# Kernel optimization log

Measured on AMD Instinct MI355X. Metric: run time of the kernel, lower is better.

The kernel has to match this reference:

```python
import jax, jax.numpy as jnp
import numpy as np

T, B, X, H, Z = 28, 16384, 28, 100, 16
EPS = 1e-10


def setup_inputs() -> dict:
    key = jax.random.key(0)
    ks = jax.random.split(key, 32)
    s = 0.1  # weight scale to keep activations sane
    d = {
        'x': jax.random.uniform(ks[0], (T, B, X), jnp.float32),
        'eps': jax.random.normal(ks[1], (T, B, Z), jnp.float32),
        'Wpx': jax.random.normal(ks[2], (H, X)) * s, 'bpx': jnp.zeros((H,)),
        'Wpz': jax.random.normal(ks[3], (H, Z)) * s, 'bpz': jnp.zeros((H,)),
        'Wp1': jax.random.normal(ks[4], (H, H)) * s, 'bp1': jnp.zeros((H,)),
        'Wp_mu': jax.random.normal(ks[5], (Z, H)) * s, 'bp_mu': jnp.zeros((Z,)),
        'Wp_sig': jax.random.normal(ks[6], (Z, H)) * s, 'bp_sig': jnp.zeros((Z,)),
        'We1': jax.random.normal(ks[7], (H, 2 * H)) * s, 'be1': jnp.zeros((H,)),
        'We_mu': jax.random.normal(ks[8], (Z, H)) * s, 'be_mu': jnp.zeros((Z,)),
        'We_sig': jax.random.normal(ks[9], (Z, H)) * s, 'be_sig': jnp.zeros((Z,)),
        'Wd1': jax.random.normal(ks[10], (H, 2 * H)) * s, 'bd1': jnp.zeros((H,)),
        'Wd2': jax.random.normal(ks[11], (H, H)) * s, 'bd2': jnp.zeros((H,)),
        'Wd3': jax.random.normal(ks[12], (X, H)) * s, 'bd3': jnp.zeros((X,)),
        'Wih': jax.random.normal(ks[13], (3 * H, 2 * H)) * s, 'Whh': jax.random.normal(ks[14], (3 * H, H)) * s,
        'bih': jnp.zeros((3 * H,)), 'bhh': jnp.zeros((3 * H,)),
    }
    return {k: v.astype(jnp.float32) for k, v in d.items()}


def _lin(a, W, b):
    return a @ W.T + b


def reference(x, eps, Wpx, bpx, Wpz, bpz, Wp1, bp1, Wp_mu, bp_mu, Wp_sig, bp_sig,
              We1, be1, We_mu, be_mu, We_sig, be_sig, Wd1, bd1, Wd2, bd2, Wd3, bd3,
              Wih, Whh, bih, bhh):
    def step(h, inp):
        xt, et = inp  # [B,X], [B,Z]
        px = jax.nn.relu(_lin(xt, Wpx, bpx))  # phi_x
        # encoder q(z|x,h)
        he = jax.nn.relu(_lin(jnp.concatenate([px, h], -1), We1, be1))
        enc_mu = _lin(he, We_mu, be_mu)
        enc_sig = jax.nn.softplus(_lin(he, We_sig, be_sig))
        # prior p(z|h)
        hp = jax.nn.relu(_lin(h, Wp1, bp1))
        pr_mu = _lin(hp, Wp_mu, bp_mu)
        pr_sig = jax.nn.softplus(_lin(hp, Wp_sig, bp_sig))
        # reparameterize (torch code uses sqrt(scale) -- treat scale as var)
        z = enc_mu + jnp.sqrt(enc_sig) * et
        pz = jax.nn.relu(_lin(z, Wpz, bpz))  # phi_z
        # decoder p(x|z,h)
        hd = jax.nn.relu(_lin(jnp.concatenate([pz, h], -1), Wd1, bd1))
        hd = jax.nn.relu(_lin(hd, Wd2, bd2))
        probs = jax.nn.sigmoid(_lin(hd, Wd3, bd3))
        # GRUCell(input=[pz, px], h)
        gi = jnp.concatenate([pz, px], -1) @ Wih.T + bih
        gh = h @ Whh.T + bhh
        ir, iu, in_ = jnp.split(gi, 3, -1)
        hr, hu, hn = jnp.split(gh, 3, -1)
        r = jax.nn.sigmoid(ir + hr)
        u = jax.nn.sigmoid(iu + hu)
        n = jnp.tanh(in_ + r * hn)
        h_next = (1.0 - u) * n + u * h
        # KL(enc || prior)
        ps = pr_sig + EPS
        kl = 0.5 * (2 * jnp.log(ps) - 2 * jnp.log(enc_sig)
                    + (enc_sig ** 2 + (enc_mu - pr_mu) ** 2) / ps ** 2 - 1.0)
        kl = kl.sum(1).mean()
        # Bernoulli NLL
        nll = -(xt * jnp.log(probs + EPS) + (1.0 - xt) * jnp.log(1.0 - probs + EPS))
        nll = nll.sum(1).mean()
        return h_next, (kl, nll)

    h0 = jnp.zeros((x.shape[1], H), x.dtype)
    _, (kls, nlls) = jax.lax.scan(step, h0, (x, eps))
    return kls.sum(), nlls.sum()
```

## Files before the change

### kernel.cpp

```cpp
#include <hip/hip_runtime.h>
#include <math.h>

#define DEVFN __device__ __forceinline__

namespace {

typedef __bf16 bf16x8 __attribute__((ext_vector_type(8)));
typedef float  f32x4  __attribute__((ext_vector_type(4)));

constexpr int T = 28, B = 16384, X = 28, H = 100, Z = 16;
constexpr int ROWS = 32;
constexpr int NTH  = 256;
constexpr int ST   = 104;
constexpr int HBUF = ROWS*ST + 24;
constexpr int XST  = 40;
constexpr float KEPS = 1e-10f;

constexpr int FB_PX   = 0;
constexpr int FB_HE   = 7;
constexpr int FB_EMU  = 63;
constexpr int FB_ESIG = 67;
constexpr int FB_HP   = 71;
constexpr int FB_PMU  = 99;
constexpr int FB_PSIG = 103;
constexpr int FB_PZ   = 107;
constexpr int FB_HD1  = 114;
constexpr int FB_HD2  = 170;
constexpr int FB_PRB  = 198;
constexpr int FB_GIR  = 206;
constexpr int FB_GIU  = 262;
constexpr int FB_GIN  = 318;
constexpr int FB_GHR  = 374;
constexpr int FB_GHU  = 402;
constexpr int FB_GHN  = 430;
constexpr int NFRAG   = 458;

struct Params {
  const float *x,*eps,*Wpx,*bpx,*Wpz,*bpz,*Wp1,*bp1,*Wp_mu,*bp_mu,*Wp_sig,*bp_sig,
              *We1,*be1,*We_mu,*be_mu,*We_sig,*be_sig,*Wd1,*bd1,*Wd2,*bd2,*Wd3,*bd3,
              *Wih,*Whh,*bih,*bhh;
  float *out;
};

DEVFN float frcp(float x){ return __builtin_amdgcn_rcpf(x); }
DEVFN float fsigmoid(float v){ return frcp(1.f + __expf(-v)); }
DEVFN float ftanh(float v){
  float t = __expf(-2.f*fabsf(v));
  float r = (1.f - t) * frcp(1.f + t);
  return copysignf(r, v);
}
DEVFN float fsoftplus(float v){
  float sp = (v > 15.f) ? v : __logf(1.f + __expf(v));
  return fmaxf(sp, 1e-6f);
}

DEVFN f32x4 MFMA(bf16x8 a, bf16x8 b, f32x4 c){
  return __builtin_amdgcn_mfma_f32_16x16x32_bf16(a, b, c, 0, 0, 0);
}

__global__ void prep_kernel(Params P, __bf16* FRW)
{
  const int f = blockIdx.x, l = threadIdx.x;
  const int bases[18] = {FB_PX,FB_HE,FB_EMU,FB_ESIG,FB_HP,FB_PMU,FB_PSIG,FB_PZ,FB_HD1,
                         FB_HD2,FB_PRB,FB_GIR,FB_GIU,FB_GIN,FB_GHR,FB_GHU,FB_GHN,NFRAG};
  int li = 0;
  while (f >= bases[li+1]) ++li;

  const float* W; const float* Bv; int KT, N, roff, wstr, vK, mode;
  switch (li) {
    case 0:  W=P.Wpx;    Bv=P.bpx;    KT=1; N=100; roff=0;   wstr=28;  vK=28;  mode=0; break;
    case 1:  W=P.We1;    Bv=P.be1;    KT=8; N=100; roff=0;   wstr=200; vK=100; mode=1; break;
    case 2:  W=P.We_mu;  Bv=P.be_mu;  KT=4; N=16;  roff=0;   wstr=100; vK=100; mode=0; break;
    case 3:  W=P.We_sig; Bv=P.be_sig; KT=4; N=16;  roff=0;   wstr=100; vK=100; mode=0; break;
    case 4:  W=P.Wp1;    Bv=P.bp1;    KT=4; N=100; roff=0;   wstr=100; vK=100; mode=0; break;
    case 5:  W=P.Wp_mu;  Bv=P.bp_mu;  KT=4; N=16;  roff=0;   wstr=100; vK=100; mode=0; break;
    case 6:  W=P.Wp_sig; Bv=P.bp_sig; KT=4; N=16;  roff=0;   wstr=100; vK=100; mode=0; break;
    case 7:  W=P.Wpz;    Bv=P.bpz;    KT=1; N=100; roff=0;   wstr=16;  vK=16;  mode=0; break;
    case 8:  W=P.Wd1;    Bv=P.bd1;    KT=8; N=100; roff=0;   wstr=200; vK=100; mode=1; break;
    case 9:  W=P.Wd2;    Bv=P.bd2;    KT=4; N=100; roff=0;   wstr=100; vK=100; mode=0; break;
    case 10: W=P.Wd3;    Bv=P.bd3;    KT=4; N=28;  roff=0;   wstr=100; vK=100; mode=0; break;
    case 11: W=P.Wih;    Bv=P.bih;    KT=8; N=100; roff=0;   wstr=200; vK=100; mode=1; break;
    case 12: W=P.Wih;    Bv=P.bih;    KT=8; N=100; roff=100; wstr=200; vK=100; mode=1; break;
    case 13: W=P.Wih;    Bv=P.bih;    KT=8; N=100; roff=200; wstr=200; vK=100; mode=1; break;
    case 14: W=P.Whh;    Bv=P.bhh;    KT=4; N=100; roff=0;   wstr=100; vK=100; mode=0; break;
    case 15: W=P.Whh;    Bv=P.bhh;    KT=4; N=100; roff=100; wstr=100; vK=100; mode=0; break;
    default: W=P.Whh;    Bv=P.bhh;    KT=4; N=100; roff=200; wstr=100; vK=100; mode=0; break;
  }
  const int idx = f - bases[li];
  const int nt = idx / KT, kc = idx % KT;
  const int n  = nt*16 + (l & 15);

  bf16x8 v;
  #pragma unroll
  for (int j = 0; j < 8; ++j) {
    int kk  = (mode ? (kc & 3) : kc)*32 + ((l >> 4)*8) + j;
    float w = 0.f;
    if (n < N) {
      if (mode == 0) {
        if (kk < vK)       w = W[(size_t)(roff + n)*wstr + kk];
        else if (kk == vK) w = Bv[roff + n];
      } else {
        int col = (kc < 4 ? 0 : 100) + kk;
        if (kk < 100)                    w = W[(size_t)(roff + n)*wstr + col];
        else if (kc < 4 && kk == 100)    w = Bv[roff + n];
      }
    }
    v[j] = (__bf16)w;
  }
  *((bf16x8*)FRW + (size_t)f*64 + l) = v;
}

template<int NC>
DEVFN void load_afrags2(bf16x8 (&af)[2][NC], const __bf16* A, int stride, int lane)
{
  #pragma unroll
  for (int mh = 0; mh < 2; ++mh) {
    const __bf16* p = A + (size_t)((lane & 15) + mh*16)*stride + ((lane >> 4)*8);
    #pragma unroll
    for (int kc = 0; kc < NC; ++kc) af[mh][kc] = *(const bf16x8*)(p + kc*32);
  }
}

DEVFN bf16x8 vload_frag(const __bf16* A, int stride, int mh, int kc, int lane)
{
  const __bf16* p = A + (size_t)((lane & 15) + mh*16)*stride + ((lane >> 4)*8) + kc*32;
  return *(const volatile bf16x8*)p;
}

template<int KT>
DEVFN void layerH2(const bf16x8 (&af)[2][KT], const bf16x8* FRbase, __bf16* dst, int sw, int step, int lane)
{
  for (int nt = sw; nt < 7; nt += step) {
    f32x4 ac0 = {0.f,0.f,0.f,0.f}, ac1 = {0.f,0.f,0.f,0.f};
    const bf16x8* wf = FRbase + (size_t)nt*KT*64 + lane;
    #pragma unroll
    for (int kc = 0; kc < KT; ++kc) {
      bf16x8 w = wf[kc*64];
      ac0 = MFMA(af[0][kc], w, ac0);
      ac1 = MFMA(af[1][kc], w, ac1);
    }
    const int col = nt*16 + (lane & 15);
    if (col < H) {
      const int rbase = (lane >> 4)*4;
      #pragma unroll
      for (int r = 0; r < 4; ++r) {
        dst[(size_t)(rbase + r)*ST + col]      = (__bf16)fmaxf(ac0[r], 0.f);
        dst[(size_t)(16 + rbase + r)*ST + col] = (__bf16)fmaxf(ac1[r], 0.f);
      }
    }
  }
}

DEVFN void layerHcat2_1(const bf16x8 (&b0)[2][4], const bf16x8 (&b1)[2][4], const bf16x8* FRbase,
                        __bf16* dst, int nt, int lane)
{
  f32x4 ac0 = {0.f,0.f,0.f,0.f}, ac1 = {0.f,0.f,0.f,0.f};
  const bf16x8* wf = FRbase + (size_t)nt*8*64 + lane;
  #pragma unroll
  for (int kc = 0; kc < 4; ++kc) {
    bf16x8 w = wf[kc*64];
    ac0 = MFMA(b0[0][kc], w, ac0);
    ac1 = MFMA(b0[1][kc], w, ac1);
  }
  #pragma unroll
  for (int kc = 0; kc < 4; ++kc) {
    bf16x8 w = wf[(4+kc)*64];
    ac0 = MFMA(b1[0][kc], w, ac0);
    ac1 = MFMA(b1[1][kc], w, ac1);
  }
  const int col = nt*16 + (lane & 15);
  if (col < H) {
    const int rbase = (lane >> 4)*4;
    #pragma unroll
    for (int r = 0; r < 4; ++r) {
      dst[(size_t)(rbase + r)*ST + col]      = (__bf16)fmaxf(ac0[r], 0.f);
      dst[(size_t)(16 + rbase + r)*ST + col] = (__bf16)fmaxf(ac1[r], 0.f);
    }
  }
}

template<int KT>
DEVFN void head4x2(const bf16x8 (&af)[2][KT], const bf16x8* FRbase, int lane, f32x4& o0, f32x4& o1)
{
  f32x4 ac0 = {0.f,0.f,0.f,0.f}, ac1 = {0.f,0.f,0.f,0.f};
  #pragma unroll
  for (int kc = 0; kc < KT; ++kc) {
    bf16x8 w = FRbase[kc*64 + lane];
    ac0 = MFMA(af[0][kc], w, ac0);
    ac1 = MFMA(af[1][kc], w, ac1);
  }
  o0 = ac0; o1 = ac1;
}

template<int KT>
DEVFN f32x4 head4(const bf16x8 (&af)[KT], const bf16x8* FRbase, int lane)
{
  f32x4 acc = {0.f,0.f,0.f,0.f};
  #pragma unroll
  for (int kc = 0; kc < KT; ++kc) acc = MFMA(af[kc], FRbase[kc*64 + lane], acc);
  return acc;
}

__global__ __launch_bounds__(NTH, 2) void vrnn_kernel(Params P, const __bf16* FRW)
{
  __shared__ alignas(16) __bf16 sPXb[2][HBUF];
  __shared__ alignas(16) __bf16 sPZ[HBUF];
  __shared__ alignas(16) __bf16 sA [HBUF];
  __shared__ alignas(16) __bf16 sBb[2][HBUF];
  __shared__ alignas(16) __bf16 sH0[HBUF];
  __shared__ alignas(16) __bf16 sH1[HBUF];
  __shared__ alignas(16) __bf16 sZ [ROWS*XST];
  __shared__ float sred[8];

  const bf16x8* FR = (const bf16x8*)FRW;
  const int tid  = threadIdx.x;
  const int lane = tid & 63;
  const int uwv  = __builtin_amdgcn_readfirstlane(tid >> 6);
  const int gr0  = blockIdx.x * ROWS;

  for (int i = tid; i < HBUF; i += NTH) {
    sPXb[0][i]=(__bf16)0.f; sPXb[1][i]=(__bf16)0.f; sPZ[i]=(__bf16)0.f; sA[i]=(__bf16)0.f;
    sBb[0][i]=(__bf16)0.f; sBb[1][i]=(__bf16)0.f; sH0[i]=(__bf16)0.f; sH1[i]=(__bf16)0.f;
  }
  for (int i = tid; i < ROWS*XST; i += NTH) sZ[i]=(__bf16)0.f;
  __syncthreads();
  if (tid < ROWS) {
    sPXb[0][tid*ST+100]=(__bf16)1.f; sPXb[1][tid*ST+100]=(__bf16)1.f;
    sPZ[tid*ST+100]=(__bf16)1.f; sA[tid*ST+100]=(__bf16)1.f;
    sBb[0][tid*ST+100]=(__bf16)1.f; sBb[1][tid*ST+100]=(__bf16)1.f;
    sH0[tid*ST+100]=(__bf16)1.f; sH1[tid*ST+100]=(__bf16)1.f;
    sZ[tid*XST+16]=(__bf16)1.f;
  }
  __syncthreads();

  float kl = 0.f, nll = 0.f;

  for (int t = 0; t < T; ++t) {
    __bf16* sHo = (t & 1) ? sH1 : sH0;
    __bf16* sHn = (t & 1) ? sH0 : sH1;
    __bf16* sPX = sPXb[t & 1];
    __bf16* sB  = sBb [t & 1];

    {
      bf16x8 ax[2][1];
      #pragma unroll
      for (int mh = 0; mh < 2; ++mh) {
        const float* xr = P.x + ((size_t)t*B + gr0 + mh*16 + (lane & 15))*X + (lane >> 4)*8;
        float4 fa = *(const float4*)xr;
        float4 fb = make_float4(0.f,0.f,0.f,0.f);
        if ((lane >> 4) < 3) fb = *(const float4*)(xr + 4);
        bf16x8 a;
        a[0]=(__bf16)fa.x; a[1]=(__bf16)fa.y; a[2]=(__bf16)fa.z; a[3]=(__bf16)fa.w;
        a[4]=(__bf16)fb.x; a[5]=(__bf16)fb.y; a[6]=(__bf16)fb.z; a[7]=(__bf16)fb.w;
        if ((lane >> 4) == 3) a[4] = (__bf16)1.f;
        ax[mh][0] = a;
      }
      layerH2<1>(ax, FR + (size_t)FB_PX*64, sPX, uwv, 4, lane);
      bf16x8 ah[2][4]; load_afrags2(ah, sHo, ST, lane);
      layerH2<4>(ah, FR + (size_t)FB_HP*64, sB, (uwv + 1) & 3, 4, lane);
    }
    __syncthreads();

    {
      bf16x8 a0[2][4]; load_afrags2(a0, sPX, ST, lane);
      bf16x8 a1[2][4]; load_afrags2(a1, sHo, ST, lane);
      for (int nt = uwv; nt < 7; nt += 4)
        layerHcat2_1(a0, a1, FR + (size_t)FB_HE*64, sA, nt, lane);
    }
    __syncthreads();

    {
      bf16x8 a1[2][4]; load_afrags2(a1, sA, ST, lane);
      bf16x8 a2[2][4]; load_afrags2(a2, sB, ST, lane);
      f32x4 emu[2], esg[2], pmu[2], psg[2];
      head4x2(a1, FR + (size_t)FB_EMU*64,  lane, emu[0], emu[1]);
      head4x2(a1, FR + (size_t)FB_ESIG*64, lane, esg[0], esg[1]);
      head4x2(a2, FR + (size_t)FB_PMU*64,  lane, pmu[0], pmu[1]);
      head4x2(a2, FR + (size_t)FB_PSIG*64, lane, psg[0], psg[1]);
      const int zi = lane & 15;
      const int rbase = (lane >> 4)*4;
      #pragma unroll
      for (int mh = 0; mh < 2; ++mh) {
        #pragma unroll
        for (int r = 0; r < 4; ++r) {
          float em = emu[mh][r];
          float es = fsoftplus(esg[mh][r]);
          float ev = P.eps[((size_t)t*B + gr0 + mh*16 + rbase + r)*Z + zi];
          sZ[(mh*16 + rbase + r)*XST + zi] = (__bf16)(em + __builtin_amdgcn_sqrtf(es)*ev);
          if (r == uwv) {
            float ps = fsoftplus(psg[mh][r]) + KEPS;
            float dm = em - pmu[mh][r];
            float rps = frcp(ps);
            kl += 0.5f*(2.f*__logf(ps*frcp(es)) + (es*es + dm*dm)*(rps*rps) - 1.f);
          }
        }
      }
    }

    {
      bf16x8 az[2][1];
      #pragma unroll
      for (int mh = 0; mh < 2; ++mh)
        az[mh][0] = *(const bf16x8*)(sZ + (size_t)((lane & 15) + mh*16)*XST + (lane >> 4)*8);
      layerH2<1>(az, FR + (size_t)FB_PZ*64, sPZ, uwv, 4, lane);
    }
    __syncthreads();

    {
      {
        bf16x8 apz[2][4]; load_afrags2(apz, sPZ, ST, lane);
        bf16x8 ah [2][4]; load_afrags2(ah,  sHo, ST, lane);
        if (uwv == 3) {
          for (int nt = 0; nt < 7; nt += 2)
            layerHcat2_1(apz, ah, FR + (size_t)FB_HD1*64, sA, nt, lane);
        } else {
          layerHcat2_1(apz, ah, FR + (size_t)FB_HD1*64, sA, 2*uwv + 1, lane);
        }
      }

      #pragma unroll 1
      for (int c = uwv; c < 7; c += 4) {
        const f32x4 z4 = {0.f,0.f,0.f,0.f};
        f32x4 gr[2]={z4,z4}, gu[2]={z4,z4}, gn[2]={z4,z4};
        const bf16x8* wr = FR + (size_t)(FB_GIR + c*8)*64 + lane;
        const bf16x8* wu = FR + (size_t)(FB_GIU + c*8)*64 + lane;
        const bf16x8* wn = FR + (size_t)(FB_GIN + c*8)*64 + lane;
        #pragma unroll
        for (int kc = 0; kc < 4; ++kc) {
          bf16x8 a0 = vload_frag(sPZ, ST, 0, kc, lane);
          bf16x8 a1 = vload_frag(sPZ, ST, 1, kc, lane);
          bf16x8 wR = wr[kc*64], wU = wu[kc*64], wN = wn[kc*64];
          gr[0] = MFMA(a0, wR, gr[0]); gu[0] = MFMA(a0, wU, gu[0]); gn[0] = MFMA(a0, wN, gn[0]);
          gr[1] = MFMA(a1, wR, gr[1]); gu[1] = MFMA(a1, wU, gu[1]); gn[1] = MFMA(a1, wN, gn[1]);
        }
        #pragma unroll
        for (int kc = 0; kc < 4; ++kc) {
          bf16x8 a0 = vload_frag(sPX, ST, 0, kc, lane);
          bf16x8 a1 = vload_frag(sPX, ST, 1, kc, lane);
          bf16x8 wR = wr[(4+kc)*64], wU = wu[(4+kc)*64], wN = wn[(4+kc)*64];
          gr[0] = MFMA(a0, wR, gr[0]); gu[0] = MFMA(a0, wU, gu[0]); gn[0] = MFMA(a0, wN, gn[0]);
          gr[1] = MFMA(a1, wR, gr[1]); gu[1] = MFMA(a1, wU, gu[1]); gn[1] = MFMA(a1, wN, gn[1]);
        }
        f32x4 hr[2]={z4,z4}, hu[2]={z4,z4}, hn[2]={z4,z4};
        const bf16x8* vr = FR + (size_t)(FB_GHR + c*4)*64 + lane;
        const bf16x8* vu = FR + (size_t)(FB_GHU + c*4)*64 + lane;
        const bf16x8* vn = FR + (size_t)(FB_GHN + c*4)*64 + lane;
        #pragma unroll
        for (int kc = 0; kc < 4; ++kc) {
          bf16x8 a0 = vload_frag(sHo, ST, 0, kc, lane);
          bf16x8 a1 = vload_frag(sHo, ST, 1, kc, lane);
          bf16x8 wR = vr[kc*64], wU = vu[kc*64], wN = vn[kc*64];
          hr[0] = MFMA(a0, wR, hr[0]); hu[0] = MFMA(a0, wU, hu[0]); hn[0] = MFMA(a0, wN, hn[0]);
          hr[1] = MFMA(a1, wR, hr[1]); hu[1] = MFMA(a1, wU, hu[1]); hn[1] = MFMA(a1, wN, hn[1]);
        }
        const int n = c*16 + (lane & 15);
        if (n < H) {
          const int rbase = (lane >> 4)*4;
          #pragma unroll
          for (int mh = 0; mh < 2; ++mh) {
            #pragma unroll
            for (int r = 0; r < 4; ++r) {
              float rr = fsigmoid(gr[mh][r] + hr[mh][r]);
              float uu = fsigmoid(gu[mh][r] + hu[mh][r]);
              float nn = ftanh(gn[mh][r] + rr*hn[mh][r]);
              const size_t off = (size_t)(mh*16 + rbase + r)*ST + n;
              float ho = (float)sHo[off];
              sHn[off] = (__bf16)((1.f-uu)*nn + uu*ho);
            }
          }
        }
      }
    }
    __syncthreads();

    {
      bf16x8 af[2][4]; load_afrags2(af, sA, ST, lane);
      layerH2<4>(af, FR + (size_t)FB_HD2*64, sB, uwv, 4, lane);
    }
    __syncthreads();

    {
      const int pt = uwv & 1;
      const int mh = uwv >> 1;
      bf16x8 af[4];
      const __bf16* p = sB + (size_t)((lane & 15) + mh*16)*ST + ((lane >> 4)*8);
      #pragma unroll
      for (int kc = 0; kc < 4; ++kc) af[kc] = *(const bf16x8*)(p + kc*32);
      f32x4 acc = head4(af, FR + (size_t)(FB_PRB + pt*4)*64, lane);
      const int n = pt*16 + (lane & 15);
      if (n < X) {
        const int rbase = (lane >> 4)*4;
        #pragma unroll
        for (int r = 0; r < 4; ++r) {
          float v  = acc[r];
          float xv = P.x[((size_t)t*B + gr0 + mh*16 + rbase + r)*X + n];
          nll += fmaxf(-v, 0.f) + __logf(1.f + __expf(-fabsf(v))) + (1.f - xv)*v;
        }
      }
    }
  }

  __syncthreads();

  for (int off = 32; off > 0; off >>= 1) {
    kl  += __shfl_down(kl,  off);
    nll += __shfl_down(nll, off);
  }
  if (lane == 0) { sred[uwv] = kl; sred[4 + uwv] = nll; }
  __syncthreads();
  if (tid == 0) {
    atomicAdd(&P.out[0], (sred[0] + sred[1] + sred[2] + sred[3]) * (1.f/(float)B));
    atomicAdd(&P.out[1], (sred[4] + sred[5] + sred[6] + sred[7]) * (1.f/(float)B));
  }
}

}

extern "C" void kernel_launch(void* const* d_in, const int* in_sizes, int n_in,
                              void* d_out, int out_size, void* d_ws, size_t ws_size,
                              hipStream_t stream)
{
  Params p;
  const float* const* f = (const float* const*)d_in;
  p.x=f[0];    p.eps=f[1];
  p.Wpx=f[2];  p.bpx=f[3];   p.Wpz=f[4];   p.bpz=f[5];
  p.Wp1=f[6];  p.bp1=f[7];   p.Wp_mu=f[8]; p.bp_mu=f[9];
  p.Wp_sig=f[10]; p.bp_sig=f[11];
  p.We1=f[12]; p.be1=f[13];  p.We_mu=f[14]; p.be_mu=f[15];
  p.We_sig=f[16]; p.be_sig=f[17];
  p.Wd1=f[18]; p.bd1=f[19];  p.Wd2=f[20];  p.bd2=f[21];
  p.Wd3=f[22]; p.bd3=f[23];
  p.Wih=f[24]; p.Whh=f[25];  p.bih=f[26];  p.bhh=f[27];
  p.out = (float*)d_out;

  hipMemsetAsync(d_out, 0, 2*sizeof(float), stream);
  prep_kernel<<<dim3(NFRAG), dim3(64), 0, stream>>>(p, (__bf16*)d_ws);
  vrnn_kernel<<<dim3(B/ROWS), dim3(NTH), 0, stream>>>(p, (const __bf16*)d_ws);
}
```

Before: 632.9 us.

## Split encoder and prior heads across waves and stage KL inputs in LDS

Before, every wave computed all four Z-heads (encoder mu/sigma and prior mu/sigma), so the same work ran four times, with each wave keeping one row slice for KL. Now wave 0 computes the encoder heads and the z sample, and wave 1 computes the prior heads. Their outputs go to a new shared buffer, and all waves later compute KL terms from it. This removes the redundant MFMA head work, at the cost of an extra __syncthreads, more LDS use, and waves 2-3 sitting idle during that phase.

```diff
diff --git a/kernel.cpp b/kernel.cpp
--- a/kernel.cpp
+++ b/kernel.cpp
@@ -14,6 +14,7 @@
 constexpr int ST   = 104;
 constexpr int HBUF = ROWS*ST + 24;
 constexpr int XST  = 40;
+constexpr int HEST = 17;
 constexpr float KEPS = 1e-10f;
 
 constexpr int FB_PX   = 0;
@@ -210,6 +211,7 @@
   __shared__ alignas(16) __bf16 sH0[HBUF];
   __shared__ alignas(16) __bf16 sH1[HBUF];
   __shared__ alignas(16) __bf16 sZ [ROWS*XST];
+  __shared__ float sHE[4*ROWS*HEST];
   __shared__ float sred[8];
 
   const bf16x8* FR = (const bf16x8*)FRW;
@@ -269,12 +271,29 @@
     }
     __syncthreads();
 
-    {
+    if (uwv == 0) {
       bf16x8 a1[2][4]; load_afrags2(a1, sA, ST, lane);
-      bf16x8 a2[2][4]; load_afrags2(a2, sB, ST, lane);
-      f32x4 emu[2], esg[2], pmu[2], psg[2];
+      f32x4 emu[2], esg[2];
       head4x2(a1, FR + (size_t)FB_EMU*64,  lane, emu[0], emu[1]);
       head4x2(a1, FR + (size_t)FB_ESIG*64, lane, esg[0], esg[1]);
+      const int zi = lane & 15;
+      const int rbase = (lane >> 4)*4;
+      #pragma unroll
+      for (int mh = 0; mh < 2; ++mh) {
+        #pragma unroll
+        for (int r = 0; r < 4; ++r) {
+          const int row = mh*16 + rbase + r;
+          float em = emu[mh][r];
+          float es = fsoftplus(esg[mh][r]);
+          float ev = P.eps[((size_t)t*B + gr0 + row)*Z + zi];
+          sZ[row*XST + zi] = (__bf16)(em + __builtin_amdgcn_sqrtf(es)*ev);
+          sHE[0*ROWS*HEST + row*HEST + zi] = em;
+          sHE[1*ROWS*HEST + row*HEST + zi] = es;
+        }
+      }
+    } else if (uwv == 1) {
+      bf16x8 a2[2][4]; load_afrags2(a2, sB, ST, lane);
+      f32x4 pmu[2], psg[2];
       head4x2(a2, FR + (size_t)FB_PMU*64,  lane, pmu[0], pmu[1]);
       head4x2(a2, FR + (size_t)FB_PSIG*64, lane, psg[0], psg[1]);
       const int zi = lane & 15;
@@ -283,19 +302,13 @@
       for (int mh = 0; mh < 2; ++mh) {
         #pragma unroll
         for (int r = 0; r < 4; ++r) {
-          float em = emu[mh][r];
-          float es = fsoftplus(esg[mh][r]);
-          float ev = P.eps[((size_t)t*B + gr0 + mh*16 + rbase + r)*Z + zi];
-          sZ[(mh*16 + rbase + r)*XST + zi] = (__bf16)(em + __builtin_amdgcn_sqrtf(es)*ev);
-          if (r == uwv) {
-            float ps = fsoftplus(psg[mh][r]) + KEPS;
-            float dm = em - pmu[mh][r];
-            float rps = frcp(ps);
-            kl += 0.5f*(2.f*__logf(ps*frcp(es)) + (es*es + dm*dm)*(rps*rps) - 1.f);
-          }
-        }
-      }
-    }
+          const int row = mh*16 + rbase + r;
+          sHE[2*ROWS*HEST + row*HEST + zi] = pmu[mh][r];
+          sHE[3*ROWS*HEST + row*HEST + zi] = fsoftplus(psg[mh][r]) + KEPS;
+        }
+      }
+    }
+    __syncthreads();
 
     {
       bf16x8 az[2][1];
@@ -307,6 +320,22 @@
     __syncthreads();
 
     {
+      {
+        const int zi = lane & 15;
+        const int r0 = 8*uwv + (lane >> 4);
+        #pragma unroll
+        for (int rr = 0; rr < 2; ++rr) {
+          const int row = r0 + rr*4;
+          float em = sHE[0*ROWS*HEST + row*HEST + zi];
+          float es = sHE[1*ROWS*HEST + row*HEST + zi];
+          float pm = sHE[2*ROWS*HEST + row*HEST + zi];
+          float ps = sHE[3*ROWS*HEST + row*HEST + zi];
+          float dm = em - pm;
+          float rps = frcp(ps);
+          kl += 0.5f*(2.f*__logf(ps*frcp(es)) + (es*es + dm*dm)*(rps*rps) - 1.f);
+        }
+      }
+
       {
         bf16x8 apz[2][4]; load_afrags2(apz, sPZ, ST, lane);
         bf16x8 ah [2][4]; load_afrags2(ah,  sHo, ST, lane);
```

Result: faster. 606.9 us, median of 2 (-4.1%).
